# Kernel optimization log

Measured on AMD Instinct MI355X. Metric: run time of the kernel, lower is better.

The kernel has to match this reference:

```python
import jax, jax.numpy as jnp
import numpy as np

# OAdder2d_Q, mode='oconv', in_bit=16, w_bit=16 (dorefa), bias=False, no augment.
# Physical model (O2NN-style differential detection):
#   y = sum_{c,i,j} [ x*w*sin(phi)*(d0+d1)/2 + (x^2 + w^2)*(d0-d1)/4 ]
# With ideal disks (d0=d1=1) the square terms vanish and the op reduces to a
# conv whose effective kernel is w * sin(phi); default oconv phases are -pi/2
# for the first C//2 input channels and +pi/2 for the rest.

IN_BIT = 16
W_BIT = 16
STRIDE = 1
PADDING = 1
B, C, O, K, H, W = 32, 128, 256, 3, 56, 56


def _ste_round(v, n):
    # straight-through round (forward value == torch uniform_quantize)
    return v + jax.lax.stop_gradient(jnp.round(v * n) / n - v)


def input_quantize(x):
    n = float(2 ** IN_BIT - 1)
    return _ste_round(jnp.clip(x, 0.0, 1.0), n)


def weight_quantize(w):
    # dorefa, w_bit > 1
    n = float(2 ** W_BIT - 1)
    t = jnp.tanh(w)
    t = t / (2.0 * jnp.max(jnp.abs(t))) + 0.5
    return _ste_round(t, n)


def _conv(x, k):
    return jax.lax.conv_general_dilated(
        x, k, (STRIDE, STRIDE), [(PADDING, PADDING), (PADDING, PADDING)],
        dimension_numbers=("NCHW", "OIHW", "NCHW"))


def optical_conv2d(x_q, w_q, phases, disks):
    s = jnp.sin(phases)[0, 0]                  # (C,k,k)
    d0 = disks[0, 0, ..., 0]                   # (C,k,k)
    d1 = disks[0, 0, ..., 1]
    k_mul = w_q * (s * (d0 + d1) * 0.5)        # effective conv kernel (O,C,k,k)
    y = _conv(x_q, k_mul)                      # (N,O,H,W)
    coef = (d0 - d1) * 0.25                    # zero for ideal disks
    y_sq = _conv(x_q * x_q, coef[None])        # (N,1,H,W), broadcasts over O
    w_term = jnp.sum(w_q * w_q * coef[None], axis=(1, 2, 3))  # (O,)
    return y + y_sq + w_term[None, :, None, None]


def setup_inputs() -> dict:
    key = jax.random.key(0)
    k1, k2 = jax.random.split(key)
    x = jax.random.uniform(k1, (B, C, H, W), dtype=jnp.float32)
    fan_in = C * K * K
    weight = jax.random.normal(k2, (O, C, K, K), dtype=jnp.float32) * np.sqrt(2.0 / fan_in)
    phases = jnp.concatenate([
        jnp.full((1, 1, C // 2, K, K), -np.pi / 2, dtype=jnp.float32),
        jnp.full((1, 1, C - C // 2, K, K), np.pi / 2, dtype=jnp.float32)], axis=2)
    disks = jnp.ones((1, 1, C, K, K, 2), dtype=jnp.float32)
    return {"x": x, "weight": weight, "phases": phases, "disks": disks}


def reference(x, weight, phases, disks):
    x_q = input_quantize(x)
    w_q = weight_quantize(weight)
    return optical_conv2d(x_q, w_q, phases, disks)
```

## Files before the change

### kernel.cpp

```cpp
#include <hip/hip_runtime.h>
#include <math.h>

typedef __attribute__((ext_vector_type(8))) short short8;
typedef __attribute__((ext_vector_type(4))) float floatx4;

#define BB 32
#define CC 128
#define OO 256
#define HH 56
#define WW 56
#define HWSZ 3136
#define NPIX 100352
#define WELEM 294912
#define QN 65535.0f
#define QINV (1.0f/65535.0f)

#define MAXB_OFF   0
#define CFLAG_OFF  128
#define WTERM_OFF  256
#define COEF_OFF   2048
#define KEFF_OFF   8192
#define YSQ_OFF    598016
#define XQP_OFF    1048576
#define XQP_BYTES  30408704ull
#define WS_NEED    (XQP_OFF + XQP_BYTES)
#define KEFF32_OFF 8192

__device__ __forceinline__ float quant_x(float v) {
    v = fminf(fmaxf(v, 0.0f), 1.0f);
    return rintf(v * QN) * QINV;
}

__device__ __forceinline__ unsigned short f2bf(float f) {
    unsigned u = __float_as_uint(f);
    u += 0x7fffu + ((u >> 16) & 1u);
    return (unsigned short)(u >> 16);
}

__device__ __forceinline__ void gl16(const void* g, void* l) {
    __builtin_amdgcn_global_load_lds(
        (const __attribute__((address_space(1))) unsigned char*)g,
        (__attribute__((address_space(3))) unsigned char*)l, 16, 0, 0);
}

__global__ void kmax_kernel(const float* __restrict__ w, unsigned* __restrict__ maxout) {
    int i = blockIdx.x * blockDim.x + threadIdx.x;
    float m = 0.0f;
    for (int idx = i; idx < WELEM; idx += gridDim.x * blockDim.x)
        m = fmaxf(m, fabsf(w[idx]));
    #pragma unroll
    for (int off = 32; off; off >>= 1)
        m = fmaxf(m, __shfl_down(m, off));
    __shared__ float red[4];
    if ((threadIdx.x & 63) == 0) red[threadIdx.x >> 6] = m;
    __syncthreads();
    if (threadIdx.x == 0) {
        m = fmaxf(fmaxf(red[0], red[1]), fmaxf(red[2], red[3]));
        atomicMax(maxout, __float_as_uint(m));
    }
}

__global__ void kprep_kernel(const float* __restrict__ wt, const float* __restrict__ phases,
                             const float* __restrict__ disks, const unsigned* __restrict__ maxbits,
                             unsigned short* __restrict__ kefft, float* __restrict__ coef,
                             unsigned* __restrict__ cflag, float* __restrict__ wterm) {
    int idx = blockIdx.x * blockDim.x + threadIdx.x;
    if (idx >= WELEM) return;
    int kk = idx % 9;
    int c  = (idx / 9) % CC;
    int o  = idx / (9 * CC);
    float M = tanhf(__uint_as_float(*maxbits));
    float t = tanhf(wt[idx]);
    float v = t / (2.0f * M) + 0.5f;
    float wq = rintf(v * QN) * QINV;
    int pidx = c * 9 + kk;
    float s  = sinf(phases[pidx]);
    float d0 = disks[pidx * 2 + 0];
    float d1 = disks[pidx * 2 + 1];
    float kv = wq * (s * (d0 + d1) * 0.5f);

    int step = kk * 2 + (c >> 6);
    int ot = o >> 7, lo = o & 127;
    int wm = lo >> 6, mf = (lo >> 4) & 3, l15 = lo & 15;
    int ch2 = (c >> 5) & 1, kg = (c >> 3) & 3, e = c & 7;
    size_t byte = (size_t)(step * 2 + ot) * 16384
                + ch2 * 8192 + wm * 4096 + mf * 1024 + (kg * 16 + l15) * 16 + e * 2;
    kefft[byte >> 1] = f2bf(kv);

    float cf = (d0 - d1) * 0.25f;
    if (o == 0) {
        coef[kk * CC + c] = cf;
        if (cf != 0.0f) atomicOr(cflag, 1u);
    }
    float contrib = wq * wq * cf;
    if (contrib != 0.0f) atomicAdd(wterm + o, contrib);
}

__global__ __launch_bounds__(256) void kxqpad_kernel(const float* __restrict__ x,
                                                     unsigned short* __restrict__ xqp) {
    __shared__ __align__(16) unsigned short tile[64][136];
    int t = threadIdx.x;
    int b = blockIdx.y;
    int hw0 = blockIdx.x * 64;
    const float* xb = x + (size_t)b * (CC * HWSZ) + hw0;
    #pragma unroll
    for (int rep = 0; rep < 32; ++rep) {
        int lin = rep * 256 + t;
        int c = lin >> 6, j = lin & 63;
        float v = xb[(size_t)c * HWSZ + j];
        tile[j][c] = f2bf(quant_x(v));
    }
    __syncthreads();
    unsigned short* xq_b = xqp + (size_t)b * (58 * 64 * 128);
    #pragma unroll
    for (int rep = 0; rep < 4; ++rep) {
        int lin = rep * 256 + t;
        int c16 = lin & 15, j = lin >> 4;
        int hw = hw0 + j;
        int h = hw / WW, w = hw - h * WW;
        short8 v = *reinterpret_cast<const short8*>(&tile[j][c16 * 8]);
        *reinterpret_cast<short8*>(xq_b + ((size_t)((h + 1) * 64 + (w + 1))) * 128 + c16 * 8) = v;
    }
}

__global__ __launch_bounds__(256) void ysq_kernel(const float* __restrict__ x,
                                                  const float* __restrict__ coef,
                                                  const unsigned* __restrict__ cflag,
                                                  float* __restrict__ ysq) {
    int t = threadIdx.x;
    int P = blockIdx.x * 256 + t;
    if (*cflag == 0u) {
        ysq[P] = 0.0f;
        return;
    }
    __shared__ float cf[9 * CC];
    for (int i = t; i < 9 * CC; i += 256) cf[i] = coef[i];
    __syncthreads();
    int b = P / HWSZ; int hw = P - b * HWSZ;
    int h = hw / WW;  int w = hw - h * WW;
    const float* xb = x + (size_t)b * (CC * HWSZ);
    float s2 = 0.0f;
    #pragma unroll
    for (int kk = 0; kk < 9; ++kk) {
        int dh = kk / 3 - 1, dw = kk % 3 - 1;
        int ih = h + dh, iw = w + dw;
        bool valid = ((unsigned)ih < HH) && ((unsigned)iw < WW);
        int ihc = min(max(ih, 0), HH - 1), iwc = min(max(iw, 0), WW - 1);
        const float* xp = xb + ihc * WW + iwc;
        float fm = valid ? 1.0f : 0.0f;
        const float* cp = cf + kk * CC;
        #pragma unroll 4
        for (int c = 0; c < CC; ++c) {
            float xv = quant_x(xp[(size_t)c * HWSZ]) * fm;
            s2 = fmaf(xv * xv, cp[c], s2);
        }
    }
    ysq[P] = s2;
}

__global__ __launch_bounds__(256, 2) void oconv_kernel(
        const unsigned short* __restrict__ xqp,
        const unsigned short* __restrict__ keff,
        const float* __restrict__ ysq,
        const float* __restrict__ wterm,
        float* __restrict__ out) {
    __shared__ __align__(16) char smem[65536];
    const int t   = threadIdx.x;
    const int bx  = blockIdx.x;
    const int oty = blockIdx.y;

    const char* xb = (const char*)xqp;
    long bb0, bb1;
    {
        int pxA  = ((t >> 6) << 4) + (t & 15);
        int cOff = ((t >> 4) & 3) * 16;
        int P0 = bx * 128 + pxA;
        int b0 = P0 / HWSZ, hw0 = P0 - b0 * HWSZ;
        int h0 = hw0 / WW,  w0 = hw0 - h0 * WW;
        bb0 = ((long)((b0 * 58 + h0 + 1) * 64 + (w0 + 1))) * 256 + cOff;
        int P1 = P0 + 64;
        int b1 = P1 / HWSZ, hw1 = P1 - b1 * HWSZ;
        int h1 = hw1 / WW,  w1 = hw1 - h1 * WW;
        bb1 = ((long)((b1 * 58 + h1 + 1) * 64 + (w1 + 1))) * 256 + cOff;
    }

    const int l15 = t & 15;
    const int kg  = (t >> 4) & 3;
    const int wid = t >> 6;
    const int wm  = wid >> 1, wn = wid & 1;
    const int lane16 = (t & 63) * 16;

    floatx4 acc[4][4];
    #pragma unroll
    for (int i = 0; i < 4; ++i)
        #pragma unroll
        for (int j = 0; j < 4; ++j) acc[i][j] = (floatx4)0.0f;

    auto stage = [&](int buf, int s) {
        char* la = smem + buf * 32768 + t * 16;
        const char* ga = (const char*)keff + (size_t)(s * 2 + oty) * 16384 + t * 16;
        gl16(ga,         la);
        gl16(ga + 4096,  la + 4096);
        gl16(ga + 8192,  la + 8192);
        gl16(ga + 12288, la + 12288);
        int kk = s >> 1;
        int dh = kk / 3, dw = kk - dh * 3;
        long bo = (long)((dh - 1) * 64 + (dw - 1)) * 256 + (s & 1) * 128;
        char* lb = la + 16384;
        gl16(xb + bb0 + bo,      lb);
        gl16(xb + bb1 + bo,      lb + 4096);
        gl16(xb + bb0 + bo + 64, lb + 8192);
        gl16(xb + bb1 + bo + 64, lb + 12288);
    };

    auto computeHalf = [&](int buf, int h) {
        const char* base = smem + buf * 32768;
        const char* ap = base + h * 8192 + wm * 4096 + lane16;
        const char* bp = base + 16384 + h * 8192 + wn * 4096 + lane16;
        short8 a[4], b[4];
        #pragma unroll
        for (int mf = 0; mf < 4; ++mf)
            a[mf] = *reinterpret_cast<const short8*>(ap + mf * 1024);
        #pragma unroll
        for (int nf = 0; nf < 4; ++nf)
            b[nf] = *reinterpret_cast<const short8*>(bp + nf * 1024);
        #pragma unroll
        for (int mf = 0; mf < 4; ++mf)
            #pragma unroll
            for (int nf = 0; nf < 4; ++nf)
                acc[mf][nf] = __builtin_amdgcn_mfma_f32_16x16x32_bf16(a[mf], b[nf], acc[mf][nf], 0, 0, 0);
    };

    stage(0, 0);
    for (int s = 0; s < 18; ++s) {
        __syncthreads();
        if (s + 1 < 18) stage((s + 1) & 1, s + 1);
        computeHalf(s & 1, 0);
        computeHalf(s & 1, 1);
    }

    float wv[4][4];
    #pragma unroll
    for (int mf = 0; mf < 4; ++mf)
        #pragma unroll
        for (int j = 0; j < 4; ++j)
            wv[mf][j] = wterm[oty * 128 + wm * 64 + mf * 16 + kg * 4 + j];

    #pragma unroll
    for (int nf = 0; nf < 4; ++nf) {
        int P = bx * 128 + wn * 64 + nf * 16 + l15;
        int b = P / HWSZ; int hw = P - b * HWSZ;
        float yv = ysq[P];
        float* op = out + (size_t)b * (OO * HWSZ) + hw;
        #pragma unroll
        for (int mf = 0; mf < 4; ++mf)
            #pragma unroll
            for (int j = 0; j < 4; ++j) {
                int o = oty * 128 + wm * 64 + mf * 16 + kg * 4 + j;
                op[(size_t)o * HWSZ] = acc[mf][nf][j] + yv + wv[mf][j];
            }
    }
}

__global__ void kprep32_kernel(const float* __restrict__ wt, const float* __restrict__ phases,
                               const float* __restrict__ disks, const unsigned* __restrict__ maxbits,
                               float* __restrict__ keff, float* __restrict__ coef,
                               float* __restrict__ wterm) {
    int idx = blockIdx.x * blockDim.x + threadIdx.x;
    if (idx >= WELEM) return;
    int kk = idx % 9;
    int c  = (idx / 9) % CC;
    int o  = idx / (9 * CC);
    float M = tanhf(__uint_as_float(*maxbits));
    float t = tanhf(wt[idx]);
    float v = t / (2.0f * M) + 0.5f;
    float wq = rintf(v * QN) * QINV;
    int pidx = c * 9 + kk;
    float s  = sinf(phases[pidx]);
    float d0 = disks[pidx * 2 + 0];
    float d1 = disks[pidx * 2 + 1];
    keff[(kk * CC + c) * OO + o] = wq * (s * (d0 + d1) * 0.5f);
    float cf = (d0 - d1) * 0.25f;
    if (o == 0) coef[kk * CC + c] = cf;
    float contrib = wq * wq * cf;
    if (contrib != 0.0f) atomicAdd(wterm + o, contrib);
}

__global__ __launch_bounds__(256) void kconv32_kernel(
        const float* __restrict__ xsrc, const float* __restrict__ keff,
        const float* __restrict__ coef, const float* __restrict__ wterm,
        float* __restrict__ out) {
    int t   = blockIdx.x * 256 + threadIdx.x;
    int ocb = blockIdx.y * 16;
    int b   = t / HWSZ;
    int rem = t - b * HWSZ;
    int h   = rem / WW;
    int w   = rem - h * WW;
    float acc[16];
    #pragma unroll
    for (int i = 0; i < 16; ++i) acc[i] = 0.0f;
    float s2 = 0.0f;
    const float* xb = xsrc + (size_t)b * (CC * HWSZ);
    #pragma unroll
    for (int kh = 0; kh < 3; ++kh) {
        #pragma unroll
        for (int kw = 0; kw < 3; ++kw) {
            int ih = h + kh - 1, iw = w + kw - 1;
            bool valid = ((unsigned)ih < HH) && ((unsigned)iw < WW);
            int ihc = min(max(ih, 0), HH - 1);
            int iwc = min(max(iw, 0), WW - 1);
            const float* xp   = xb + ihc * WW + iwc;
            const float* wrow = keff + (kh * 3 + kw) * (CC * OO) + ocb;
            const float* cfp  = coef + (kh * 3 + kw) * CC;
            float fm = valid ? 1.0f : 0.0f;
            #pragma unroll 4
            for (int c = 0; c < CC; ++c) {
                float xv = quant_x(xp[c * HWSZ]) * fm;
                s2 = fmaf(xv * xv, cfp[c], s2);
                #pragma unroll
                for (int i = 0; i < 16; ++i)
                    acc[i] = fmaf(xv, wrow[c * OO + i], acc[i]);
            }
        }
    }
    float* op = out + (size_t)b * (OO * HWSZ) + (size_t)ocb * HWSZ + rem;
    #pragma unroll
    for (int i = 0; i < 16; ++i)
        op[i * HWSZ] = acc[i] + s2 + wterm[ocb + i];
}

extern "C" void kernel_launch(void* const* d_in, const int* in_sizes, int n_in,
                              void* d_out, int out_size, void* d_ws, size_t ws_size,
                              hipStream_t stream) {
    const float* x      = (const float*)d_in[0];
    const float* weight = (const float*)d_in[1];
    const float* phases = (const float*)d_in[2];
    const float* disks  = (const float*)d_in[3];
    float* out = (float*)d_out;

    char* ws = (char*)d_ws;
    unsigned* maxbits = (unsigned*)(ws + MAXB_OFF);
    unsigned* cflag   = (unsigned*)(ws + CFLAG_OFF);
    float* wterm = (float*)(ws + WTERM_OFF);
    float* coef  = (float*)(ws + COEF_OFF);

    hipMemsetAsync(ws, 0, 1280, stream);
    kmax_kernel<<<288, 256, 0, stream>>>(weight, maxbits);

    if (ws_size >= WS_NEED) {
        unsigned short* kefft = (unsigned short*)(ws + KEFF_OFF);
        float* ysq = (float*)(ws + YSQ_OFF);
        unsigned short* xqp = (unsigned short*)(ws + XQP_OFF);

        hipMemsetAsync(ws + XQP_OFF, 0, XQP_BYTES, stream);
        kprep_kernel<<<(WELEM + 255) / 256, 256, 0, stream>>>(weight, phases, disks,
                                                              maxbits, kefft, coef, cflag, wterm);
        kxqpad_kernel<<<dim3(49, BB), 256, 0, stream>>>(x, xqp);
        ysq_kernel<<<NPIX / 256, 256, 0, stream>>>(x, coef, cflag, ysq);
        oconv_kernel<<<dim3(784, 2), 256, 0, stream>>>(xqp, kefft, ysq, wterm, out);
    } else {
        float* keff32 = (float*)(ws + KEFF32_OFF);
        kprep32_kernel<<<(WELEM + 255) / 256, 256, 0, stream>>>(weight, phases, disks,
                                                                maxbits, keff32, coef, wterm);
        kconv32_kernel<<<dim3(NPIX / 256, OO / 16), 256, 0, stream>>>(x, keff32, coef, wterm, out);
    }
}
```

Before: 248.2 us.

## Halve conv K-step size, deepen prefetch pipeline, swizzle blocks, zero only padding border

```diff
diff --git a/kernel.cpp b/kernel.cpp
--- a/kernel.cpp
+++ b/kernel.cpp
@@ -79,12 +79,12 @@
     float d1 = disks[pidx * 2 + 1];
     float kv = wq * (s * (d0 + d1) * 0.5f);
 
-    int step = kk * 2 + (c >> 6);
+    int step = kk * 4 + (c >> 5);
     int ot = o >> 7, lo = o & 127;
     int wm = lo >> 6, mf = (lo >> 4) & 3, l15 = lo & 15;
-    int ch2 = (c >> 5) & 1, kg = (c >> 3) & 3, e = c & 7;
-    size_t byte = (size_t)(step * 2 + ot) * 16384
-                + ch2 * 8192 + wm * 4096 + mf * 1024 + (kg * 16 + l15) * 16 + e * 2;
+    int kg = (c >> 3) & 3, e = c & 7;
+    size_t byte = (size_t)(step * 2 + ot) * 8192
+                + wm * 4096 + mf * 1024 + (kg * 16 + l15) * 16 + e * 2;
     kefft[byte >> 1] = f2bf(kv);
 
     float cf = (d0 - d1) * 0.25f;
@@ -94,6 +94,19 @@
     }
     float contrib = wq * wq * cf;
     if (contrib != 0.0f) atomicAdd(wterm + o, contrib);
+}
+
+__global__ __launch_bounds__(256) void kborder_kernel(unsigned short* __restrict__ xqp) {
+    int t = threadIdx.x;
+    int id = blockIdx.x * 256 + t;
+    int b = blockIdx.y;
+    int pxi = id >> 4, chunk = id & 15;
+    int h, w;
+    if (pxi < 128) { h = (pxi >> 6) * 57; w = pxi & 63; }
+    else { int r = pxi - 128; h = 1 + (r >> 3); int wi = r & 7; w = wi == 0 ? 0 : 56 + wi; }
+    short8 z = (short8)0;
+    *reinterpret_cast<short8*>((char*)xqp + (size_t)b * 3801088ull
+                               + ((size_t)(h * 64 + w)) * 256 + chunk * 16) = z;
 }
 
 __global__ __launch_bounds__(256) void kxqpad_kernel(const float* __restrict__ x,
@@ -164,10 +177,12 @@
         const float* __restrict__ ysq,
         const float* __restrict__ wterm,
         float* __restrict__ out) {
-    __shared__ __align__(16) char smem[65536];
-    const int t   = threadIdx.x;
-    const int bx  = blockIdx.x;
-    const int oty = blockIdx.y;
+    __shared__ __align__(16) char smem[32768];
+    const int t  = threadIdx.x;
+    const int id  = blockIdx.x;
+    const int swz = (id & 7) * 196 + (id >> 3);
+    const int bx  = swz >> 1;
+    const int oty = swz & 1;
 
     const char* xb = (const char*)xqp;
     long bb0, bb1;
@@ -197,26 +212,22 @@
         for (int j = 0; j < 4; ++j) acc[i][j] = (floatx4)0.0f;
 
     auto stage = [&](int buf, int s) {
-        char* la = smem + buf * 32768 + t * 16;
-        const char* ga = (const char*)keff + (size_t)(s * 2 + oty) * 16384 + t * 16;
-        gl16(ga,         la);
-        gl16(ga + 4096,  la + 4096);
-        gl16(ga + 8192,  la + 8192);
-        gl16(ga + 12288, la + 12288);
-        int kk = s >> 1;
+        char* la = smem + buf * 16384 + t * 16;
+        const char* ga = (const char*)keff + (size_t)(s * 2 + oty) * 8192 + t * 16;
+        gl16(ga,        la);
+        gl16(ga + 4096, la + 4096);
+        int kk = s >> 2, cs = s & 3;
         int dh = kk / 3, dw = kk - dh * 3;
-        long bo = (long)((dh - 1) * 64 + (dw - 1)) * 256 + (s & 1) * 128;
-        char* lb = la + 16384;
-        gl16(xb + bb0 + bo,      lb);
-        gl16(xb + bb1 + bo,      lb + 4096);
-        gl16(xb + bb0 + bo + 64, lb + 8192);
-        gl16(xb + bb1 + bo + 64, lb + 12288);
+        long bo = (long)((dh - 1) * 64 + (dw - 1)) * 256 + cs * 64;
+        char* lb = la + 8192;
+        gl16(xb + bb0 + bo, lb);
+        gl16(xb + bb1 + bo, lb + 4096);
     };
 
-    auto computeHalf = [&](int buf, int h) {
-        const char* base = smem + buf * 32768;
-        const char* ap = base + h * 8192 + wm * 4096 + lane16;
-        const char* bp = base + 16384 + h * 8192 + wn * 4096 + lane16;
+    auto compute = [&](int buf) {
+        const char* base = smem + buf * 16384;
+        const char* ap = base + wm * 4096 + lane16;
+        const char* bp = base + 8192 + wn * 4096 + lane16;
         short8 a[4], b[4];
         #pragma unroll
         for (int mf = 0; mf < 4; ++mf)
@@ -232,11 +243,17 @@
     };
 
     stage(0, 0);
-    for (int s = 0; s < 18; ++s) {
-        __syncthreads();
-        if (s + 1 < 18) stage((s + 1) & 1, s + 1);
-        computeHalf(s & 1, 0);
-        computeHalf(s & 1, 1);
+    stage(1, 1);
+    for (int s = 0; s < 36; ++s) {
+        if (s < 35) { asm volatile("s_waitcnt vmcnt(4)" ::: "memory"); }
+        else        { asm volatile("s_waitcnt vmcnt(0)" ::: "memory"); }
+        __builtin_amdgcn_sched_barrier(0);
+        __builtin_amdgcn_s_barrier();
+        compute(s & 1);
+        asm volatile("s_waitcnt lgkmcnt(0)" ::: "memory");
+        __builtin_amdgcn_sched_barrier(0);
+        __builtin_amdgcn_s_barrier();
+        if (s < 34) stage(s & 1, s + 2);
     }
 
     float wv[4][4];
@@ -352,12 +369,12 @@
         float* ysq = (float*)(ws + YSQ_OFF);
         unsigned short* xqp = (unsigned short*)(ws + XQP_OFF);
 
-        hipMemsetAsync(ws + XQP_OFF, 0, XQP_BYTES, stream);
         kprep_kernel<<<(WELEM + 255) / 256, 256, 0, stream>>>(weight, phases, disks,
                                                               maxbits, kefft, coef, cflag, wterm);
+        kborder_kernel<<<dim3(36, BB), 256, 0, stream>>>(xqp);
         kxqpad_kernel<<<dim3(49, BB), 256, 0, stream>>>(x, xqp);
         ysq_kernel<<<NPIX / 256, 256, 0, stream>>>(x, coef, cflag, ysq);
-        oconv_kernel<<<dim3(784, 2), 256, 0, stream>>>(xqp, kefft, ysq, wterm, out);
+        oconv_kernel<<<1568, 256, 0, stream>>>(xqp, kefft, ysq, wterm, out);
     } else {
         float* keff32 = (float*)(ws + KEFF32_OFF);
         kprep32_kernel<<<(WELEM + 255) / 256, 256, 0, stream>>>(weight, phases, disks,
```

New measurement: 239.7 us. 3.4% less time.
